# Kernel optimization log

Measured on AMD Instinct MI355X. Metric: run time of the kernel, lower is better.

The kernel has to match this reference:

```python
import jax, jax.numpy as jnp
import numpy as np

HID = 512; NH = 8; FEAT = 128; NCELLS = 64; NGRAPHS = 64; NODES_PER = 64; DEG = 16
SCALE = 0.02


def setup_inputs() -> dict:
    key = jax.random.key(0)
    ks = iter(jax.random.split(key, 32))
    counts_np = 2 + (np.arange(NCELLS) % 7)              # genes per cell, 2..8
    G = int(counts_np.sum())                              # 317 total genes
    cell_ids_np = np.repeat(np.arange(NCELLS), counts_np)
    rank_np = np.concatenate([np.arange(c) for c in counts_np])
    Lmax = int(counts_np.max()) * NGRAPHS                 # padded per-cell seq len
    N = NGRAPHS * NODES_PER
    E = N * DEG
    rn = lambda k, s: jax.random.normal(k, s, dtype=jnp.float32) * SCALE
    inp = {
        'x': jax.random.normal(next(ks), (N, FEAT), dtype=jnp.float32),
        'edge_index': jax.random.randint(next(ks), (2, E), 0, N, dtype=jnp.int32),
        'batch': jnp.repeat(jnp.arange(NGRAPHS, dtype=jnp.int32), NODES_PER),
        'gene_W': rn(next(ks), (G, FEAT, HID)),
        'gene_b': jnp.zeros((G, HID), jnp.float32),
        'cell_ids': jnp.asarray(cell_ids_np, jnp.int32),
        'rank': jnp.asarray(rank_np, jnp.int32),
        'counts': jnp.asarray(counts_np, jnp.int32),
        'Wq': rn(next(ks), (HID, HID)), 'bq': jnp.zeros((HID,), jnp.float32),
        'Wk': rn(next(ks), (HID, HID)), 'bk': jnp.zeros((HID,), jnp.float32),
        'Wv': rn(next(ks), (HID, HID)), 'bv': jnp.zeros((HID,), jnp.float32),
        'Wo': rn(next(ks), (HID, HID)), 'bo': jnp.zeros((HID,), jnp.float32),
        'Wi1': rn(next(ks), (HID, 2 * HID)), 'bi1': jnp.zeros((2 * HID,), jnp.float32),
        'Wi2': rn(next(ks), (2 * HID, HID)), 'bi2': jnp.zeros((HID,), jnp.float32),
        'ln_g': jnp.ones((HID,), jnp.float32), 'ln_b': jnp.zeros((HID,), jnp.float32),
        'Aw1': rn(next(ks), (NCELLS, HID, HID)), 'Ab1': jnp.zeros((NCELLS, HID), jnp.float32),
        'Aw2': rn(next(ks), (NCELLS, HID)), 'Ab2': jnp.zeros((NCELLS,), jnp.float32),
        'Lmax': Lmax,
        'num_graphs': NGRAPHS,
    }
    return inp


def reference(x, edge_index, batch, gene_W, gene_b, cell_ids, rank, counts,
              Wq, bq, Wk, bk, Wv, bv, Wo, bo,
              Wi1, bi1, Wi2, bi2, ln_g, ln_b,
              Aw1, Ab1, Aw2, Ab2, Lmax, num_graphs):
    N = x.shape[0]; H = Wq.shape[0]; nh = NH; dh = H // nh
    C = counts.shape[0]; B = num_graphs
    # --- gene GNN: one-hop mean aggregation + per-graph mean pool + per-gene Linear/ReLU ---
    src, dst = edge_index[0], edge_index[1]
    deg = jax.ops.segment_sum(jnp.ones((src.shape[0],), x.dtype), dst, num_segments=N)
    agg = jax.ops.segment_sum(x[src], dst, num_segments=N)
    xn = x + agg / jnp.maximum(deg, 1.0)[:, None]
    gsum = jax.ops.segment_sum(xn, batch, num_segments=B)
    gcnt = jax.ops.segment_sum(jnp.ones((N,), x.dtype), batch, num_segments=B)
    pooled = gsum / gcnt[:, None]                                  # [B, F]
    gene_out = jax.nn.relu(jnp.einsum('bf,gfh->gbh', pooled, gene_W) + gene_b[:, None, :])  # [G,B,H]
    # --- ragged regroup: rows of gene g go to cell cell_ids[g] at positions rank[g]*B + b ---
    pos = rank[:, None] * B + jnp.arange(B)[None, :]               # [G, B]
    padded = jnp.zeros((C, Lmax, H), x.dtype).at[cell_ids[:, None], pos].set(gene_out)
    seqlen = counts * B                                            # valid length per cell
    valid = jnp.arange(Lmax)[None, :] < seqlen[:, None]            # [C, Lmax]
    # --- shared multi-head self-attention over each cell's gene rows (key padding mask) ---
    q = (padded @ Wq + bq).reshape(C, Lmax, nh, dh)
    k = (padded @ Wk + bk).reshape(C, Lmax, nh, dh)
    v = (padded @ Wv + bv).reshape(C, Lmax, nh, dh)
    scores = jnp.einsum('clhd,cmhd->chlm', q, k) * (1.0 / np.sqrt(dh))
    scores = jnp.where(valid[:, None, None, :], scores, -1e9)
    attn = jax.nn.softmax(scores, axis=-1)
    attended = jnp.einsum('chlm,cmhd->clhd', attn, v).reshape(C, Lmax, H) @ Wo + bo
    vf = valid.astype(x.dtype)
    meanh = (attended * vf[:, :, None]).sum(axis=1) / seqlen[:, None].astype(x.dtype)  # [C,H]
    # --- shared integrator: Linear -> ReLU -> (Dropout=eval identity) -> Linear -> LayerNorm ---
    h = jax.nn.relu(meanh @ Wi1 + bi1) @ Wi2 + bi2
    mu = h.mean(-1, keepdims=True)
    var = ((h - mu) ** 2).mean(-1, keepdims=True)
    integrated = (h - mu) / jnp.sqrt(var + 1e-5) * ln_g + ln_b     # [C, H]
    # --- per-cell affinity heads ---
    h1 = jax.nn.relu(jnp.einsum('ch,chk->ck', integrated, Aw1) + Ab1)
    aff = jax.nn.sigmoid(jnp.einsum('ck,ck->c', h1, Aw2) + Ab2)
    return aff[:, None], integrated[:, None, :]
```

## Files before the change

kernel.cpp:

```cpp
#include <hip/hip_runtime.h>
#include <hip/hip_bf16.h>
#include <math.h>

#define NNODES 4096
#define NEDGES 65536
#define NFEAT  128
#define NPG    64
#define NG     317
#define NB     64
#define H      512
#define DH     64
#define NROWS  20288

typedef __attribute__((ext_vector_type(8))) short short8v;
typedef __attribute__((ext_vector_type(4))) float float4v;

#define WS_DEG    0u
#define WS_AGG    4096u
#define WS_POOLED 528384u
#define WS_ROWSB  536576u
#define WS_WT     5730304u
#define WS_QB     6123520u
#define WS_KB     11317248u
#define WS_VB     16510976u
#define WS_CTX    21704704u
#define WS_MEANH  21737472u
#define WS_TMP1   21770240u

__device__ __forceinline__ float bf2f(ushort u) {
    union { unsigned int i; float f; } x; x.i = ((unsigned int)u) << 16; return x.f;
}

__global__ void deg_kernel(const int* __restrict__ ei, float* __restrict__ deg) {
    int e = blockIdx.x * 256 + threadIdx.x;
    atomicAdd(&deg[ei[NEDGES + e]], 1.0f);
}

__global__ void agg_kernel(const int* __restrict__ ei, const float* __restrict__ x,
                           float* __restrict__ agg) {
    int idx = blockIdx.x * 256 + threadIdx.x;
    int e = idx >> 5, f4 = idx & 31;
    int s = ei[e], d = ei[NEDGES + e];
    float4 v = ((const float4*)x)[s * 32 + f4];
    float* a = &agg[d * NFEAT + f4 * 4];
    atomicAdd(a + 0, v.x);
    atomicAdd(a + 1, v.y);
    atomicAdd(a + 2, v.z);
    atomicAdd(a + 3, v.w);
}

__global__ void pooled_kernel(const float* __restrict__ x, const float* __restrict__ agg,
                              const float* __restrict__ deg, float* __restrict__ pooled) {
    int b = blockIdx.x, f = threadIdx.x;
    float s = 0.f;
    for (int i = 0; i < NPG; ++i) {
        int n = b * NPG + i;
        s += x[n * NFEAT + f] + agg[n * NFEAT + f] / fmaxf(deg[n], 1.0f);
    }
    pooled[b * NFEAT + f] = s * (1.0f / 64.0f);
}

__global__ __launch_bounds__(512) void gene_kernel(const float* __restrict__ pooled,
        const float* __restrict__ gW, const float* __restrict__ gb, ushort* __restrict__ rowsb) {
    __shared__ float ps[NB * NFEAT];
    int g = blockIdx.x, t = threadIdx.x;
    for (int i = t; i < NB * NFEAT; i += 512) ps[i] = pooled[i];
    __syncthreads();
    float acc[NB];
    #pragma unroll
    for (int b = 0; b < NB; ++b) acc[b] = 0.f;
    const float* wp = &gW[g * NFEAT * H + t];
    for (int f4 = 0; f4 < NFEAT; f4 += 4) {
        float w0 = wp[(f4 + 0) * H], w1 = wp[(f4 + 1) * H];
        float w2 = wp[(f4 + 2) * H], w3 = wp[(f4 + 3) * H];
        #pragma unroll
        for (int b = 0; b < NB; ++b) {
            float4 p = *(const float4*)&ps[b * NFEAT + f4];
            acc[b] += p.x * w0 + p.y * w1 + p.z * w2 + p.w * w3;
        }
    }
    float bias = gb[g * H + t];
    #pragma unroll
    for (int b = 0; b < NB; ++b) {
        float val = fmaxf(acc[b] + bias, 0.f);
        __hip_bfloat16 bv = __float2bfloat16(val);
        rowsb[(g * NB + b) * H + t] = *(ushort*)&bv;
    }
}

__global__ void wcvt_kernel(const float* __restrict__ Wq, const float* __restrict__ Wk,
                            const float* __restrict__ Wv, ushort* __restrict__ WT) {
    __shared__ float tile[32][33];
    int z = blockIdx.z;
    const float* W = z == 0 ? Wq : (z == 1 ? Wk : Wv);
    ushort* out = WT + (size_t)z * H * H;
    int k0 = blockIdx.x * 32, n0 = blockIdx.y * 32;
    int tx = threadIdx.x, ty = threadIdx.y;
    for (int j = 0; j < 32; j += 8)
        tile[ty + j][tx] = W[(size_t)(k0 + ty + j) * H + n0 + tx];
    __syncthreads();
    for (int j = 0; j < 32; j += 8) {
        __hip_bfloat16 b = __float2bfloat16(tile[tx][ty + j]);
        out[(size_t)(n0 + ty + j) * H + k0 + tx] = *(ushort*)&b;
    }
}

__global__ __launch_bounds__(256) void qkv_mfma(const ushort* __restrict__ rowsb,
        const ushort* __restrict__ WT,
        const float* __restrict__ bq, const float* __restrict__ bk, const float* __restrict__ bv,
        ushort* __restrict__ q, ushort* __restrict__ k, ushort* __restrict__ v) {
    __shared__ ushort As[64][40];
    __shared__ ushort Bs[256][40];
    int z = blockIdx.z;
    const ushort* w = WT + (size_t)z * H * H;
    const float* bias = z == 0 ? bq : (z == 1 ? bk : bv);
    ushort* out = z == 0 ? q : (z == 1 ? k : v);
    int m0 = blockIdx.x * 64, n0 = blockIdx.y * 256;
    int t = threadIdx.x;
    int wave = t >> 6, lane = t & 63;
    int fr = lane & 15, fk = (lane >> 4) * 8;
    float4v acc[4][4] = {};
    int r = t >> 2, seg = t & 3;
    for (int k0 = 0; k0 < H; k0 += 32) {
        uint4 av = *(const uint4*)&rowsb[(size_t)(m0 + r) * H + k0 + seg * 8];
        uint4 bvv[4];
        #pragma unroll
        for (int i = 0; i < 4; ++i)
            bvv[i] = *(const uint4*)&w[(size_t)(n0 + r + i * 64) * H + k0 + seg * 8];
        __syncthreads();
        *(uint4*)&As[r][seg * 8] = av;
        #pragma unroll
        for (int i = 0; i < 4; ++i)
            *(uint4*)&Bs[r + i * 64][seg * 8] = bvv[i];
        __syncthreads();
        short8v af[4], bf[4];
        #pragma unroll
        for (int mi = 0; mi < 4; ++mi) af[mi] = *(const short8v*)&As[mi * 16 + fr][fk];
        #pragma unroll
        for (int ni = 0; ni < 4; ++ni) bf[ni] = *(const short8v*)&Bs[wave * 64 + ni * 16 + fr][fk];
        #pragma unroll
        for (int mi = 0; mi < 4; ++mi)
            #pragma unroll
            for (int ni = 0; ni < 4; ++ni)
                acc[mi][ni] = __builtin_amdgcn_mfma_f32_16x16x32_bf16(af[mi], bf[ni], acc[mi][ni], 0, 0, 0);
    }
    int fq = lane >> 4;
    #pragma unroll
    for (int ni = 0; ni < 4; ++ni) {
        int col = n0 + wave * 64 + ni * 16 + fr;
        float bb = bias[col];
        #pragma unroll
        for (int mi = 0; mi < 4; ++mi) {
            #pragma unroll
            for (int rr = 0; rr < 4; ++rr) {
                int row = m0 + mi * 16 + fq * 4 + rr;
                __hip_bfloat16 bvv = __float2bfloat16(acc[mi][ni][rr] + bb);
                out[(size_t)row * H + col] = *(ushort*)&bvv;
            }
        }
    }
}

__global__ __launch_bounds__(64) void attn_kernel(const ushort* __restrict__ q,
        const ushort* __restrict__ k, const ushort* __restrict__ v,
        const int* __restrict__ counts, float* __restrict__ ctx) {
    __shared__ float w_lds[64];
    int qt = blockIdx.x, h = blockIdx.y, c = blockIdx.z;
    int cnt = counts[c];
    if (qt * 32 >= cnt * 64) return;
    int cs = 0;
    for (int i = 0; i < c; ++i) cs += counts[i];
    int lane = threadIdx.x;
    int fr = lane & 15, fkb = (lane >> 4) * 8;
    size_t rowbase = (size_t)(cs * 64) * H + (size_t)h * DH;
    const ushort* qp = q + rowbase + (size_t)(qt * 32) * H;
    const ushort* kp = k + rowbase;
    const ushort* vp = v + rowbase;
    short8v qf[2][2];
    #pragma unroll
    for (int mi = 0; mi < 2; ++mi)
        #pragma unroll
        for (int s = 0; s < 2; ++s)
            qf[mi][s] = *(const short8v*)&qp[(size_t)(mi * 16 + fr) * H + s * 32 + fkb];
    float4v dacc[2] = {};
    for (int kt = 0; kt < cnt; ++kt) {
        const ushort* kpt = kp + (size_t)(kt * 64) * H;
        short8v kf[4][2];
        #pragma unroll
        for (int n = 0; n < 4; ++n)
            #pragma unroll
            for (int s = 0; s < 2; ++s)
                kf[n][s] = *(const short8v*)&kpt[(size_t)(n * 16 + fr) * H + s * 32 + fkb];
        #pragma unroll
        for (int mi = 0; mi < 2; ++mi) {
            #pragma unroll
            for (int n = 0; n < 4; ++n) {
                float4v acc = {};
                acc = __builtin_amdgcn_mfma_f32_16x16x32_bf16(qf[mi][0], kf[n][0], acc, 0, 0, 0);
                acc = __builtin_amdgcn_mfma_f32_16x16x32_bf16(qf[mi][1], kf[n][1], acc, 0, 0, 0);
                #pragma unroll
                for (int rr = 0; rr < 4; ++rr)
                    dacc[mi][rr] += __expf(acc[rr] * 0.125f);
            }
        }
    }
    #pragma unroll
    for (int off = 1; off < 16; off <<= 1) {
        #pragma unroll
        for (int mi = 0; mi < 2; ++mi)
            #pragma unroll
            for (int rr = 0; rr < 4; ++rr)
                dacc[mi][rr] += __shfl_xor(dacc[mi][rr], off, 64);
    }
    float4v invd[2];
    #pragma unroll
    for (int mi = 0; mi < 2; ++mi)
        #pragma unroll
        for (int rr = 0; rr < 4; ++rr)
            invd[mi][rr] = 1.0f / dacc[mi][rr];
    float o0 = 0.f, o1 = 0.f, o2 = 0.f, o3 = 0.f;
    for (int kt = 0; kt < cnt; ++kt) {
        const ushort* kpt = kp + (size_t)(kt * 64) * H;
        short8v kf[4][2];
        #pragma unroll
        for (int n = 0; n < 4; ++n)
            #pragma unroll
            for (int s = 0; s < 2; ++s)
                kf[n][s] = *(const short8v*)&kpt[(size_t)(n * 16 + fr) * H + s * 32 + fkb];
        float wpart[4] = {0.f, 0.f, 0.f, 0.f};
        #pragma unroll
        for (int mi = 0; mi < 2; ++mi) {
            #pragma unroll
            for (int n = 0; n < 4; ++n) {
                float4v acc = {};
                acc = __builtin_amdgcn_mfma_f32_16x16x32_bf16(qf[mi][0], kf[n][0], acc, 0, 0, 0);
                acc = __builtin_amdgcn_mfma_f32_16x16x32_bf16(qf[mi][1], kf[n][1], acc, 0, 0, 0);
                #pragma unroll
                for (int rr = 0; rr < 4; ++rr)
                    wpart[n] += __expf(acc[rr] * 0.125f) * invd[mi][rr];
            }
        }
        #pragma unroll
        for (int n = 0; n < 4; ++n) {
            wpart[n] += __shfl_xor(wpart[n], 16, 64);
            wpart[n] += __shfl_xor(wpart[n], 32, 64);
        }
        if (lane < 16) {
            #pragma unroll
            for (int n = 0; n < 4; ++n) w_lds[n * 16 + lane] = wpart[n];
        }
        __syncthreads();
        const ushort* vrow = vp + (size_t)(kt * 64) * H;
        #pragma unroll 4
        for (int key = 0; key < 64; key += 4) {
            float w0 = w_lds[key + 0], w1 = w_lds[key + 1];
            float w2 = w_lds[key + 2], w3 = w_lds[key + 3];
            o0 += w0 * bf2f(vrow[(size_t)(key + 0) * H + lane]);
            o1 += w1 * bf2f(vrow[(size_t)(key + 1) * H + lane]);
            o2 += w2 * bf2f(vrow[(size_t)(key + 2) * H + lane]);
            o3 += w3 * bf2f(vrow[(size_t)(key + 3) * H + lane]);
        }
        __syncthreads();
    }
    atomicAdd(&ctx[c * H + h * DH + lane], (o0 + o1) + (o2 + o3));
}

__global__ __launch_bounds__(512) void meanh_kernel(const float* __restrict__ ctx,
        const float* __restrict__ Wo, const float* __restrict__ bo,
        const int* __restrict__ counts, float* __restrict__ meanh) {
    __shared__ float cs[H];
    int c = blockIdx.x, j = threadIdx.x;
    cs[j] = ctx[c * H + j];
    __syncthreads();
    float acc = 0.f;
    for (int i = 0; i < H; ++i) acc += cs[i] * Wo[i * H + j];
    meanh[c * H + j] = acc / (float)(counts[c] * 64) + bo[j];
}

__global__ __launch_bounds__(1024) void ff1_kernel(const float* __restrict__ meanh,
        const float* __restrict__ Wi1, const float* __restrict__ bi1, float* __restrict__ tmp1) {
    __shared__ float ms[H];
    int c = blockIdx.x, j = threadIdx.x;
    if (j < H) ms[j] = meanh[c * H + j];
    __syncthreads();
    float acc = 0.f;
    for (int i = 0; i < H; ++i) acc += ms[i] * Wi1[i * 1024 + j];
    tmp1[c * 1024 + j] = fmaxf(acc + bi1[j], 0.f);
}

__device__ __forceinline__ float block_sum512(float val, float* red8) {
    #pragma unroll
    for (int off = 32; off; off >>= 1) val += __shfl_xor(val, off, 64);
    int w = threadIdx.x >> 6;
    if ((threadIdx.x & 63) == 0) red8[w] = val;
    __syncthreads();
    float s = red8[0] + red8[1] + red8[2] + red8[3] + red8[4] + red8[5] + red8[6] + red8[7];
    __syncthreads();
    return s;
}

__global__ __launch_bounds__(512) void final_kernel(const float* __restrict__ tmp1,
        const float* __restrict__ Wi2, const float* __restrict__ bi2,
        const float* __restrict__ ln_g, const float* __restrict__ ln_b,
        const float* __restrict__ Aw1, const float* __restrict__ Ab1,
        const float* __restrict__ Aw2, const float* __restrict__ Ab2,
        float* __restrict__ out) {
    __shared__ float t1[1024];
    __shared__ float integ_s[H];
    __shared__ float red8[8];
    int c = blockIdx.x, j = threadIdx.x;
    t1[j] = tmp1[c * 1024 + j];
    t1[j + 512] = tmp1[c * 1024 + j + 512];
    __syncthreads();
    float acc = 0.f;
    for (int i = 0; i < 1024; ++i) acc += t1[i] * Wi2[i * H + j];
    float hval = acc + bi2[j];
    float mu = block_sum512(hval, red8) * (1.0f / 512.0f);
    float d = hval - mu;
    float var = block_sum512(d * d, red8) * (1.0f / 512.0f);
    float integ = d * rsqrtf(var + 1e-5f) * ln_g[j] + ln_b[j];
    out[64 + c * H + j] = integ;
    integ_s[j] = integ;
    __syncthreads();
    float acc2 = 0.f;
    const float* A1 = &Aw1[(size_t)c * H * H];
    for (int i = 0; i < H; ++i) acc2 += integ_s[i] * A1[i * H + j];
    float h1 = fmaxf(acc2 + Ab1[c * H + j], 0.f);
    float part = h1 * Aw2[c * H + j];
    float tot = block_sum512(part, red8);
    if (j == 0) out[c] = 1.0f / (1.0f + __expf(-(tot + Ab2[c])));
}

extern "C" void kernel_launch(void* const* d_in, const int* in_sizes, int n_in,
                              void* d_out, int out_size, void* d_ws, size_t ws_size,
                              hipStream_t stream) {
    const float* x      = (const float*)d_in[0];
    const int*   ei     = (const int*)d_in[1];
    const float* gene_W = (const float*)d_in[3];
    const float* gene_b = (const float*)d_in[4];
    const int*   counts = (const int*)d_in[7];
    const float* Wq = (const float*)d_in[8];  const float* bq = (const float*)d_in[9];
    const float* Wk = (const float*)d_in[10]; const float* bk = (const float*)d_in[11];
    const float* Wv = (const float*)d_in[12]; const float* bv = (const float*)d_in[13];
    const float* Wo = (const float*)d_in[14]; const float* bo = (const float*)d_in[15];
    const float* Wi1 = (const float*)d_in[16]; const float* bi1 = (const float*)d_in[17];
    const float* Wi2 = (const float*)d_in[18]; const float* bi2 = (const float*)d_in[19];
    const float* ln_g = (const float*)d_in[20]; const float* ln_b = (const float*)d_in[21];
    const float* Aw1 = (const float*)d_in[22]; const float* Ab1 = (const float*)d_in[23];
    const float* Aw2 = (const float*)d_in[24]; const float* Ab2 = (const float*)d_in[25];
    float* ws = (float*)d_ws;
    float* outp = (float*)d_out;
    ushort* rowsb = (ushort*)(ws + WS_ROWSB);
    ushort* WT    = (ushort*)(ws + WS_WT);
    ushort* qb    = (ushort*)(ws + WS_QB);
    ushort* kb    = (ushort*)(ws + WS_KB);
    ushort* vb    = (ushort*)(ws + WS_VB);

    hipMemsetAsync(ws + WS_DEG, 0, (size_t)WS_POOLED * sizeof(float), stream);
    hipMemsetAsync(ws + WS_CTX, 0, (size_t)32768 * sizeof(float), stream);

    deg_kernel<<<NEDGES / 256, 256, 0, stream>>>(ei, ws + WS_DEG);
    agg_kernel<<<NEDGES * 32 / 256, 256, 0, stream>>>(ei, x, ws + WS_AGG);
    pooled_kernel<<<NB, NFEAT, 0, stream>>>(x, ws + WS_AGG, ws + WS_DEG, ws + WS_POOLED);
    gene_kernel<<<NG, 512, 0, stream>>>(ws + WS_POOLED, gene_W, gene_b, rowsb);
    wcvt_kernel<<<dim3(16, 16, 3), dim3(32, 8), 0, stream>>>(Wq, Wk, Wv, WT);
    qkv_mfma<<<dim3(NROWS / 64, 2, 3), 256, 0, stream>>>(rowsb, WT, bq, bk, bv, qb, kb, vb);
    attn_kernel<<<dim3(16, 8, 64), 64, 0, stream>>>(qb, kb, vb, counts, ws + WS_CTX);
    meanh_kernel<<<NB, H, 0, stream>>>(ws + WS_CTX, Wo, bo, counts, ws + WS_MEANH);
    ff1_kernel<<<NB, 1024, 0, stream>>>(ws + WS_MEANH, Wi1, bi1, ws + WS_TMP1);
    final_kernel<<<NB, H, 0, stream>>>(ws + WS_TMP1, Wi2, bi2, ln_g, ln_b,
        Aw1, Ab1, Aw2, Ab2, outp);
}
```

Before: 820.7 us.

## Retile QKV GEMM to 128x128 with prefetch, split gene and affinity kernels

The QKV MFMA GEMM moves from 64x256 tiles with a K step of 32 to 128x128 tiles with a K step of 64. It uses a 2x2 wave layout and register prefetch of the next K slice, and all three projections are folded into a single N dimension of 1536. The gene kernel is split into two 256-thread halves along the hidden dimension, and the per-cell affinity matvec is split into four K slices reduced with atomics. The aim is better operand reuse, hidden global latency, and more parallel blocks for kernels that previously ran only 64 or 317 blocks. The cost is extra kernel launches, atomic traffic, padded or clamped rows in the last M tile, and a larger workspace memset.

```diff
diff --git a/kernel.cpp b/kernel.cpp
--- a/kernel.cpp
+++ b/kernel.cpp
@@ -11,6 +11,7 @@
 #define H      512
 #define DH     64
 #define NROWS  20288
+#define MPAD   20352
 
 typedef __attribute__((ext_vector_type(8))) short short8v;
 typedef __attribute__((ext_vector_type(4))) float float4v;
@@ -21,11 +22,13 @@
 #define WS_ROWSB  536576u
 #define WS_WT     5730304u
 #define WS_QB     6123520u
-#define WS_KB     11317248u
-#define WS_VB     16510976u
-#define WS_CTX    21704704u
-#define WS_MEANH  21737472u
-#define WS_TMP1   21770240u
+#define WS_KB     11333632u
+#define WS_VB     16543744u
+#define WS_CTX    21753856u
+#define WS_HAFF   21786624u
+#define WS_MEANH  21819392u
+#define WS_TMP1   21852160u
+#define WS_INTEG  21917696u
 
 __device__ __forceinline__ float bf2f(ushort u) {
     union { unsigned int i; float f; } x; x.i = ((unsigned int)u) << 16; return x.f;
@@ -60,16 +63,17 @@
     pooled[b * NFEAT + f] = s * (1.0f / 64.0f);
 }
 
-__global__ __launch_bounds__(512) void gene_kernel(const float* __restrict__ pooled,
+__global__ __launch_bounds__(256) void gene_kernel(const float* __restrict__ pooled,
         const float* __restrict__ gW, const float* __restrict__ gb, ushort* __restrict__ rowsb) {
     __shared__ float ps[NB * NFEAT];
     int g = blockIdx.x, t = threadIdx.x;
-    for (int i = t; i < NB * NFEAT; i += 512) ps[i] = pooled[i];
+    int h = blockIdx.y * 256 + t;
+    for (int i = t; i < NB * NFEAT; i += 256) ps[i] = pooled[i];
     __syncthreads();
     float acc[NB];
     #pragma unroll
     for (int b = 0; b < NB; ++b) acc[b] = 0.f;
-    const float* wp = &gW[g * NFEAT * H + t];
+    const float* wp = &gW[(size_t)g * NFEAT * H + h];
     for (int f4 = 0; f4 < NFEAT; f4 += 4) {
         float w0 = wp[(f4 + 0) * H], w1 = wp[(f4 + 1) * H];
         float w2 = wp[(f4 + 2) * H], w3 = wp[(f4 + 3) * H];
@@ -79,12 +83,12 @@
             acc[b] += p.x * w0 + p.y * w1 + p.z * w2 + p.w * w3;
         }
     }
-    float bias = gb[g * H + t];
+    float bias = gb[g * H + h];
     #pragma unroll
     for (int b = 0; b < NB; ++b) {
         float val = fmaxf(acc[b] + bias, 0.f);
         __hip_bfloat16 bv = __float2bfloat16(val);
-        rowsb[(g * NB + b) * H + t] = *(ushort*)&bv;
+        rowsb[(size_t)(g * NB + b) * H + h] = *(ushort*)&bv;
     }
 }
 
@@ -109,53 +113,75 @@
         const ushort* __restrict__ WT,
         const float* __restrict__ bq, const float* __restrict__ bk, const float* __restrict__ bv,
         ushort* __restrict__ q, ushort* __restrict__ k, ushort* __restrict__ v) {
-    __shared__ ushort As[64][40];
-    __shared__ ushort Bs[256][40];
-    int z = blockIdx.z;
-    const ushort* w = WT + (size_t)z * H * H;
+    __shared__ ushort As[128][68];
+    __shared__ ushort Bs[128][68];
+    int nt = blockIdx.x, mt = blockIdx.y;
+    int m0 = mt * 128;
+    int n0g = nt * 128;
+    int z = n0g >> 9;
+    int n0 = n0g & 511;
     const float* bias = z == 0 ? bq : (z == 1 ? bk : bv);
     ushort* out = z == 0 ? q : (z == 1 ? k : v);
-    int m0 = blockIdx.x * 64, n0 = blockIdx.y * 256;
     int t = threadIdx.x;
     int wave = t >> 6, lane = t & 63;
-    int fr = lane & 15, fk = (lane >> 4) * 8;
+    int wr = wave >> 1, wc = wave & 1;
+    int fr = lane & 15, fq = lane >> 4;
+    int srow = t >> 1, shalf = t & 1;
+    int grow = m0 + srow; grow = grow < NROWS ? grow : NROWS - 1;
+    const ushort* gaBase = &rowsb[(size_t)grow * H + shalf * 32];
+    const ushort* gbBase = &WT[(size_t)(n0g + srow) * H + shalf * 32];
     float4v acc[4][4] = {};
-    int r = t >> 2, seg = t & 3;
-    for (int k0 = 0; k0 < H; k0 += 32) {
-        uint4 av = *(const uint4*)&rowsb[(size_t)(m0 + r) * H + k0 + seg * 8];
-        uint4 bvv[4];
-        #pragma unroll
-        for (int i = 0; i < 4; ++i)
-            bvv[i] = *(const uint4*)&w[(size_t)(n0 + r + i * 64) * H + k0 + seg * 8];
+    uint4 ar[4], br[4];
+    #pragma unroll
+    for (int i = 0; i < 4; ++i) {
+        ar[i] = *(const uint4*)(gaBase + i * 8);
+        br[i] = *(const uint4*)(gbBase + i * 8);
+    }
+    for (int kt = 0; kt < 8; ++kt) {
         __syncthreads();
-        *(uint4*)&As[r][seg * 8] = av;
-        #pragma unroll
-        for (int i = 0; i < 4; ++i)
-            *(uint4*)&Bs[r + i * 64][seg * 8] = bvv[i];
+        #pragma unroll
+        for (int i = 0; i < 4; ++i) {
+            *(uint4*)&As[srow][shalf * 32 + i * 8] = ar[i];
+            *(uint4*)&Bs[srow][shalf * 32 + i * 8] = br[i];
+        }
         __syncthreads();
-        short8v af[4], bf[4];
-        #pragma unroll
-        for (int mi = 0; mi < 4; ++mi) af[mi] = *(const short8v*)&As[mi * 16 + fr][fk];
-        #pragma unroll
-        for (int ni = 0; ni < 4; ++ni) bf[ni] = *(const short8v*)&Bs[wave * 64 + ni * 16 + fr][fk];
-        #pragma unroll
-        for (int mi = 0; mi < 4; ++mi)
+        if (kt < 7) {
+            int k0n = (kt + 1) * 64;
+            #pragma unroll
+            for (int i = 0; i < 4; ++i) {
+                ar[i] = *(const uint4*)(gaBase + k0n + i * 8);
+                br[i] = *(const uint4*)(gbBase + k0n + i * 8);
+            }
+        }
+        #pragma unroll
+        for (int s2 = 0; s2 < 2; ++s2) {
+            short8v af[4], bf[4];
+            #pragma unroll
+            for (int mi = 0; mi < 4; ++mi)
+                af[mi] = *(const short8v*)&As[wr * 64 + mi * 16 + fr][s2 * 32 + fq * 8];
             #pragma unroll
             for (int ni = 0; ni < 4; ++ni)
-                acc[mi][ni] = __builtin_amdgcn_mfma_f32_16x16x32_bf16(af[mi], bf[ni], acc[mi][ni], 0, 0, 0);
-    }
-    int fq = lane >> 4;
-    #pragma unroll
-    for (int ni = 0; ni < 4; ++ni) {
-        int col = n0 + wave * 64 + ni * 16 + fr;
-        float bb = bias[col];
-        #pragma unroll
-        for (int mi = 0; mi < 4; ++mi) {
-            #pragma unroll
-            for (int rr = 0; rr < 4; ++rr) {
-                int row = m0 + mi * 16 + fq * 4 + rr;
-                __hip_bfloat16 bvv = __float2bfloat16(acc[mi][ni][rr] + bb);
-                out[(size_t)row * H + col] = *(ushort*)&bvv;
+                bf[ni] = *(const short8v*)&Bs[wc * 64 + ni * 16 + fr][s2 * 32 + fq * 8];
+            #pragma unroll
+            for (int mi = 0; mi < 4; ++mi)
+                #pragma unroll
+                for (int ni = 0; ni < 4; ++ni)
+                    acc[mi][ni] = __builtin_amdgcn_mfma_f32_16x16x32_bf16(af[mi], bf[ni], acc[mi][ni], 0, 0, 0);
+        }
+    }
+    float bcol[4];
+    #pragma unroll
+    for (int ni = 0; ni < 4; ++ni) bcol[ni] = bias[n0 + wc * 64 + ni * 16 + fr];
+    #pragma unroll
+    for (int mi = 0; mi < 4; ++mi) {
+        #pragma unroll
+        for (int rr = 0; rr < 4; ++rr) {
+            size_t rbase = (size_t)(m0 + wr * 64 + mi * 16 + fq * 4 + rr) * H;
+            #pragma unroll
+            for (int ni = 0; ni < 4; ++ni) {
+                int col = n0 + wc * 64 + ni * 16 + fr;
+                __hip_bfloat16 b = __float2bfloat16(acc[mi][ni][rr] + bcol[ni]);
+                out[rbase + col] = *(ushort*)&b;
             }
         }
     }
@@ -299,14 +325,11 @@
     return s;
 }
 
-__global__ __launch_bounds__(512) void final_kernel(const float* __restrict__ tmp1,
+__global__ __launch_bounds__(512) void ln_kernel(const float* __restrict__ tmp1,
         const float* __restrict__ Wi2, const float* __restrict__ bi2,
         const float* __restrict__ ln_g, const float* __restrict__ ln_b,
-        const float* __restrict__ Aw1, const float* __restrict__ Ab1,
-        const float* __restrict__ Aw2, const float* __restrict__ Ab2,
-        float* __restrict__ out) {
+        float* __restrict__ integ_out, float* __restrict__ out) {
     __shared__ float t1[1024];
-    __shared__ float integ_s[H];
     __shared__ float red8[8];
     int c = blockIdx.x, j = threadIdx.x;
     t1[j] = tmp1[c * 1024 + j];
@@ -320,12 +343,27 @@
     float var = block_sum512(d * d, red8) * (1.0f / 512.0f);
     float integ = d * rsqrtf(var + 1e-5f) * ln_g[j] + ln_b[j];
     out[64 + c * H + j] = integ;
-    integ_s[j] = integ;
-    __syncthreads();
-    float acc2 = 0.f;
-    const float* A1 = &Aw1[(size_t)c * H * H];
-    for (int i = 0; i < H; ++i) acc2 += integ_s[i] * A1[i * H + j];
-    float h1 = fmaxf(acc2 + Ab1[c * H + j], 0.f);
+    integ_out[c * H + j] = integ;
+}
+
+__global__ __launch_bounds__(512) void affin1_kernel(const float* __restrict__ integ,
+        const float* __restrict__ Aw1, float* __restrict__ haff) {
+    __shared__ float is[128];
+    int c = blockIdx.x, sl = blockIdx.y, j = threadIdx.x;
+    if (j < 128) is[j] = integ[c * H + sl * 128 + j];
+    __syncthreads();
+    const float* A1 = Aw1 + (size_t)c * H * H + (size_t)sl * 128 * H;
+    float acc = 0.f;
+    for (int i = 0; i < 128; ++i) acc += is[i] * A1[i * H + j];
+    atomicAdd(&haff[c * H + j], acc);
+}
+
+__global__ __launch_bounds__(512) void affin2_kernel(const float* __restrict__ haff,
+        const float* __restrict__ Ab1, const float* __restrict__ Aw2,
+        const float* __restrict__ Ab2, float* __restrict__ out) {
+    __shared__ float red8[8];
+    int c = blockIdx.x, j = threadIdx.x;
+    float h1 = fmaxf(haff[c * H + j] + Ab1[c * H + j], 0.f);
     float part = h1 * Aw2[c * H + j];
     float tot = block_sum512(part, red8);
     if (j == 0) out[c] = 1.0f / (1.0f + __expf(-(tot + Ab2[c])));
@@ -357,17 +395,19 @@
     ushort* vb    = (ushort*)(ws + WS_VB);
 
     hipMemsetAsync(ws + WS_DEG, 0, (size_t)WS_POOLED * sizeof(float), stream);
-    hipMemsetAsync(ws + WS_CTX, 0, (size_t)32768 * sizeof(float), stream);
+    hipMemsetAsync(ws + WS_CTX, 0, (size_t)65536 * sizeof(float), stream);
 
     deg_kernel<<<NEDGES / 256, 256, 0, stream>>>(ei, ws + WS_DEG);
     agg_kernel<<<NEDGES * 32 / 256, 256, 0, stream>>>(ei, x, ws + WS_AGG);
     pooled_kernel<<<NB, NFEAT, 0, stream>>>(x, ws + WS_AGG, ws + WS_DEG, ws + WS_POOLED);
-    gene_kernel<<<NG, 512, 0, stream>>>(ws + WS_POOLED, gene_W, gene_b, rowsb);
+    gene_kernel<<<dim3(NG, 2), 256, 0, stream>>>(ws + WS_POOLED, gene_W, gene_b, rowsb);
     wcvt_kernel<<<dim3(16, 16, 3), dim3(32, 8), 0, stream>>>(Wq, Wk, Wv, WT);
-    qkv_mfma<<<dim3(NROWS / 64, 2, 3), 256, 0, stream>>>(rowsb, WT, bq, bk, bv, qb, kb, vb);
+    qkv_mfma<<<dim3(12, 159), 256, 0, stream>>>(rowsb, WT, bq, bk, bv, qb, kb, vb);
     attn_kernel<<<dim3(16, 8, 64), 64, 0, stream>>>(qb, kb, vb, counts, ws + WS_CTX);
     meanh_kernel<<<NB, H, 0, stream>>>(ws + WS_CTX, Wo, bo, counts, ws + WS_MEANH);
     ff1_kernel<<<NB, 1024, 0, stream>>>(ws + WS_MEANH, Wi1, bi1, ws + WS_TMP1);
-    final_kernel<<<NB, H, 0, stream>>>(ws + WS_TMP1, Wi2, bi2, ln_g, ln_b,
-        Aw1, Ab1, Aw2, Ab2, outp);
-}
+    ln_kernel<<<NB, H, 0, stream>>>(ws + WS_TMP1, Wi2, bi2, ln_g, ln_b,
+        ws + WS_INTEG, outp);
+    affin1_kernel<<<dim3(NB, 4), H, 0, stream>>>(ws + WS_INTEG, Aw1, ws + WS_HAFF);
+    affin2_kernel<<<NB, H, 0, stream>>>(ws + WS_HAFF, Ab1, Aw2, Ab2, outp);
+}
```

Result: faster. 798.9 us (-2.7%).
